# Optimization experiments

Measured on AMD Instinct MI355X. Metric: run time of the kernel, lower is better.

The kernel has to match this reference:

```python
import jax, jax.numpy as jnp
import numpy as np

NUM_EXPERTS = 8
TOP_K = 2
IN_C, HID, OUT_C, R_C = 192, 384, 192, 8
B, H, W = 4, 128, 128


def setup_inputs() -> dict:
    key = jax.random.key(0)
    ks = jax.random.split(key, 12)
    s = 0.05
    return {
        "x": jax.random.normal(ks[0], (B, IN_C, H, W), jnp.float32),
        "router_input": jax.random.normal(ks[1], (B, R_C, H, W), jnp.float32),
        "router_W": jax.random.normal(ks[2], (NUM_EXPERTS, R_C), jnp.float32) * s,
        "router_b": jnp.zeros((NUM_EXPERTS,), jnp.float32),
        "W1": jax.random.normal(ks[3], (NUM_EXPERTS, HID, IN_C), jnp.float32) * s,
        "b1": jnp.zeros((NUM_EXPERTS, HID), jnp.float32),
        "W2": jax.random.normal(ks[4], (NUM_EXPERTS, HID, HID), jnp.float32) * s,
        "b2": jnp.zeros((NUM_EXPERTS, HID), jnp.float32),
        "W3": jax.random.normal(ks[5], (NUM_EXPERTS, OUT_C, HID), jnp.float32) * (s * 0.1),
        "b3": jnp.zeros((NUM_EXPERTS, OUT_C), jnp.float32),
    }


def _gates(router_input, router_W, router_b):
    # logits: (B, E, H, W) via 1x1 conv == per-pixel linear
    logits = jnp.einsum('ec,bchw->behw', router_W, router_input) + router_b[None, :, None, None]
    lt = jnp.moveaxis(logits, 1, -1)                      # (B,H,W,E)
    _, idx = jax.lax.top_k(lt, TOP_K)                     # (B,H,W,K)
    onehot = jax.nn.one_hot(idx, NUM_EXPERTS, dtype=bool).any(axis=-2)  # (B,H,W,E)
    masked = jnp.where(onehot, lt, -jnp.inf)
    gates = jax.nn.softmax(masked, axis=-1)               # (B,H,W,E)
    return jnp.moveaxis(gates, -1, 1)                     # (B,E,H,W)


def reference(x, router_input, router_W, router_b, W1, b1, W2, b2, W3, b3):
    gates = _gates(router_input, router_W, router_b)      # (B,E,H,W)
    out = jnp.zeros((x.shape[0], OUT_C) + x.shape[2:], x.dtype)
    gelu = lambda t: jax.nn.gelu(t, approximate=False)    # torch nn.GELU is exact
    for e in range(NUM_EXPERTS):
        h1 = gelu(jnp.einsum('oc,bchw->bohw', W1[e], x) + b1[e][None, :, None, None])
        h2 = gelu(jnp.einsum('oc,bchw->bohw', W2[e], h1) + b2[e][None, :, None, None])
        y = jnp.einsum('oc,bchw->bohw', W3[e], h2) + b3[e][None, :, None, None]
        out = out + gates[:, e:e + 1] * y
    return out
```

## Files before the change

kernel.cpp:

```cpp
#include <hip/hip_runtime.h>
#include <math.h>

#define NE 8
#define IN_C 192
#define HID 384
#define OUT_C 192
#define R_C 8
#define HW 16384
#define NPIX 65536
#define PPB 16384
#define TNP 128

typedef _Float16 h8_t __attribute__((ext_vector_type(8)));
typedef float f32x4 __attribute__((ext_vector_type(4)));

__device__ __forceinline__ float gelu_exact(float v) {
  float z  = v * 0.70710678118654752f;
  float az = fabsf(z);
  float t  = __builtin_amdgcn_rcpf(1.0f + 0.3275911f * az);
  float p  = ((((1.061405429f * t - 1.453152027f) * t + 1.421413741f) * t
               - 0.284496736f) * t + 0.254829592f) * t;
  float er = 1.0f - p * __expf(-z * z);
  er = copysignf(er, z);
  return 0.5f * v * (1.0f + er);
}

__global__ __launch_bounds__(256) void router_kernel(
    const float* __restrict__ rin, const float* __restrict__ rW,
    const float* __restrict__ rb, int* __restrict__ counts,
    int* __restrict__ lists, float* __restrict__ gatev) {
  const int tid = threadIdx.x;
  const int pid = blockIdx.x * 256 + tid;
  const int img = pid >> 14;
  const int p = pid & (PPB - 1);

  __shared__ int lcount[NE];
  __shared__ int lbase[NE];
  if (tid < NE) lcount[tid] = 0;
  __syncthreads();

  const float* rbase = rin + (size_t)img * R_C * HW + p;
  float r[R_C];
#pragma unroll
  for (int c = 0; c < R_C; ++c) r[c] = rbase[(size_t)c * HW];
  float lg[NE];
#pragma unroll
  for (int e = 0; e < NE; ++e) {
    float s = rb[e];
#pragma unroll
    for (int c = 0; c < R_C; ++c) s += rW[e * R_C + c] * r[c];
    lg[e] = s;
  }
  int e0 = 0; float l0 = lg[0];
#pragma unroll
  for (int e = 1; e < NE; ++e) { if (lg[e] > l0) { l0 = lg[e]; e0 = e; } }
  int e1 = -1; float l1 = -3.4e38f;
#pragma unroll
  for (int e = 0; e < NE; ++e) {
    if (e != e0 && lg[e] > l1) { l1 = lg[e]; e1 = e; }
  }
  float ex  = expf(l1 - l0);
  float inv = 1.0f / (1.0f + ex);
  float g0 = inv, g1 = ex * inv;

  int pos0 = atomicAdd(&lcount[e0], 1);
  int pos1 = atomicAdd(&lcount[e1], 1);
  __syncthreads();
  if (tid < NE) lbase[tid] = atomicAdd(&counts[tid * 4 + img], lcount[tid]);
  __syncthreads();

  int i0 = (e0 * 4 + img) * PPB + lbase[e0] + pos0;
  lists[i0] = p;
  gatev[i0] = g0;
  int i1 = (e1 * 4 + img) * PPB + lbase[e1] + pos1;
  lists[i1] = p | (1 << 14);
  gatev[i1] = g1;
}

__global__ __launch_bounds__(256) void cvt_w1(const float* __restrict__ W,
                                              _Float16* __restrict__ d) {
  int t = blockIdx.x * 256 + threadIdx.x;
  const int QE = 73728 / 4;
  if (t >= NE * QE) return;
  int e = t / QE, q = t % QE;
  int j4 = q & 1; q >>= 1;
  int m = q % 192; q /= 192;
  int g = q % 4;   q /= 4;
  int c = q % 6;   q /= 6;
  int h = q;
  int row = h * 192 + m, col = 32 * c + 8 * g + 4 * j4;
  float4 v = *(const float4*)(W + (size_t)e * 73728 + (size_t)row * 192 + col);
  union { _Float16 h4[4]; uint2 u; } cv;
  cv.h4[0] = (_Float16)v.x; cv.h4[1] = (_Float16)v.y;
  cv.h4[2] = (_Float16)v.z; cv.h4[3] = (_Float16)v.w;
  ((uint2*)d)[t] = cv.u;
}

__global__ __launch_bounds__(256) void cvt_w2(const float* __restrict__ W,
                                              _Float16* __restrict__ d) {
  int t = blockIdx.x * 256 + threadIdx.x;
  const int QE = 147456 / 4;
  if (t >= NE * QE) return;
  int e = t / QE, q = t % QE;
  int j4 = q & 1; q >>= 1;
  int m = q % 192; q /= 192;
  int g = q % 4;   q /= 4;
  int mh = q % 2;  q /= 2;
  int c = q % 6;   q /= 6;
  int kh = q;
  int row = mh * 192 + m;
  int col = kh * 192 + 32 * c + 8 * g + 4 * j4;
  float4 v = *(const float4*)(W + (size_t)e * 147456 + (size_t)row * 384 + col);
  union { _Float16 h4[4]; uint2 u; } cv;
  cv.h4[0] = (_Float16)v.x; cv.h4[1] = (_Float16)v.y;
  cv.h4[2] = (_Float16)v.z; cv.h4[3] = (_Float16)v.w;
  ((uint2*)d)[t] = cv.u;
}

__global__ __launch_bounds__(256) void cvt_w3(const float* __restrict__ W,
                                              _Float16* __restrict__ d) {
  int t = blockIdx.x * 256 + threadIdx.x;
  const int QE = 73728 / 4;
  if (t >= NE * QE) return;
  int e = t / QE, q = t % QE;
  int j4 = q & 1; q >>= 1;
  int m = q % 192; q /= 192;
  int g = q % 4;   q /= 4;
  int c = q;
  int col = 32 * c + 8 * g + 4 * j4;
  float4 v = *(const float4*)(W + (size_t)e * 73728 + (size_t)m * 384 + col);
  union { _Float16 h4[4]; uint2 u; } cv;
  cv.h4[0] = (_Float16)v.x; cv.h4[1] = (_Float16)v.y;
  cv.h4[2] = (_Float16)v.z; cv.h4[3] = (_Float16)v.w;
  ((uint2*)d)[t] = cv.u;
}

__global__ __launch_bounds__(256) void xt_kernel(const float* __restrict__ x,
                                                 _Float16* __restrict__ xt, int pair) {
  const int img2 = blockIdx.y;
  const float* xb = x + (size_t)(pair * 2 + img2) * IN_C * HW;
  _Float16* dst = xt + (size_t)img2 * PPB * 192;
  const int tid = threadIdx.x;
  const int p = blockIdx.x * 64 + (tid & 63);
  const int cq0 = tid >> 6;
#pragma unroll
  for (int cq = 0; cq < 6; ++cq) {
    int chq = cq * 4 + cq0;
    union { _Float16 h[8]; uint4 u; } pk;
#pragma unroll
    for (int j = 0; j < 8; ++j)
      pk.h[j] = (_Float16)xb[(size_t)(chq * 8 + j) * HW + p];
    *(uint4*)(dst + (size_t)p * 192 + chq * 8) = pk.u;
  }
}

__device__ __forceinline__ void stage16(const _Float16* __restrict__ src,
                                        char* lds, int tid) {
  const int wid = tid >> 6;
  const char* g = (const char*)src;
  __builtin_amdgcn_global_load_lds(
      (const __attribute__((address_space(1))) void*)(g + tid * 16),
      (__attribute__((address_space(3))) void*)(lds + wid * 1024), 16, 0, 0);
  if (wid < 4)
    __builtin_amdgcn_global_load_lds(
        (const __attribute__((address_space(1))) void*)(g + 8192 + tid * 16),
        (__attribute__((address_space(3))) void*)(lds + 8192 + wid * 1024), 16, 0, 0);
}

__device__ __forceinline__ void pwait(int wid, bool last) {
  if (last)          asm volatile("s_waitcnt vmcnt(0)");
  else if (wid < 4)  asm volatile("s_waitcnt vmcnt(2)");
  else               asm volatile("s_waitcnt vmcnt(1)");
  __builtin_amdgcn_sched_barrier(0);
  __builtin_amdgcn_s_barrier();
  __builtin_amdgcn_sched_barrier(0);
}

__device__ __forceinline__ const _Float16* chunk_src(
    const _Float16* W1e, const _Float16* W2e, const _Float16* W3e, int cg) {
  if (cg < 6)  return W1e + cg * 6144;
  if (cg < 18) return W2e + (cg - 6) * 6144;
  if (cg < 24) return W1e + 36864 + (cg - 18) * 6144;
  if (cg < 36) return W2e + 73728 + (cg - 24) * 6144;
  return W3e + (cg - 36) * 6144;
}

template <int NM, int NT>
__device__ __forceinline__ void mfma_chunk(const _Float16* __restrict__ A,
                                           const _Float16* __restrict__ B, int kb4,
                                           int m0, int nt0,
                                           f32x4 (&acc)[NM][NT], int lane) {
  const int l15 = lane & 15, g = lane >> 4;
  h8_t a[NM], b[NT];
#pragma unroll
  for (int i = 0; i < NM; ++i)
    a[i] = *(const h8_t*)(A + ((size_t)g * 192 + m0 + i * 16 + l15) * 8);
#pragma unroll
  for (int t = 0; t < NT; ++t)
    b[t] = *(const h8_t*)(B + (((size_t)(kb4 + g) * TNP) + (nt0 + t) * 16 + l15) * 8);
#pragma unroll
  for (int i = 0; i < NM; ++i)
#pragma unroll
    for (int t = 0; t < NT; ++t)
      acc[i][t] = __builtin_amdgcn_mfma_f32_16x16x32_f16(a[i], b[t], acc[i][t], 0, 0, 0);
}

template <int NM, int NT>
__device__ __forceinline__ void act_store(f32x4 (&acc)[NM][NT], const float* __restrict__ bias,
                                          _Float16* __restrict__ Dst, int m0, int nt0, int lane) {
  const int l15 = lane & 15, g = lane >> 4;
#pragma unroll
  for (int i = 0; i < NM; ++i) {
    int rb = m0 + i * 16 + 4 * g;
    float4 bv = *(const float4*)(bias + rb);
#pragma unroll
    for (int t = 0; t < NT; ++t) {
      int n = (nt0 + t) * 16 + l15;
      union { _Float16 h[4]; uint2 u; } cv;
      cv.h[0] = (_Float16)gelu_exact(acc[i][t][0] + bv.x);
      cv.h[1] = (_Float16)gelu_exact(acc[i][t][1] + bv.y);
      cv.h[2] = (_Float16)gelu_exact(acc[i][t][2] + bv.z);
      cv.h[3] = (_Float16)gelu_exact(acc[i][t][3] + bv.w);
      *(uint2*)(Dst + (((size_t)(rb >> 3) * TNP) + n) * 8 + (rb & 7)) = cv.u;
    }
  }
}

template <int NM, int NT>
__device__ __forceinline__ void ybuf_store(f32x4 (&acc)[NM][NT], const float* __restrict__ bias,
                                           _Float16* __restrict__ ybuf,
                                           const int* __restrict__ pidsl,
                                           const float* __restrict__ pg,
                                           int npt, int m0, int nt0, int lane) {
  const int l15 = lane & 15, g = lane >> 4;
#pragma unroll
  for (int t = 0; t < NT; ++t) {
    int n = (nt0 + t) * 16 + l15;
    if (n >= npt) continue;
    float gt = pg[n];
    _Float16* yb = ybuf + pidsl[n];
#pragma unroll
    for (int i = 0; i < NM; ++i) {
      int rb = m0 + i * 16 + 4 * g;
      float4 bv = *(const float4*)(bias + rb);
      union { _Float16 h[4]; uint2 u; } cv;
      cv.h[0] = (_Float16)((acc[i][t][0] + bv.x) * gt);
      cv.h[1] = (_Float16)((acc[i][t][1] + bv.y) * gt);
      cv.h[2] = (_Float16)((acc[i][t][2] + bv.z) * gt);
      cv.h[3] = (_Float16)((acc[i][t][3] + bv.w) * gt);
      *(uint2*)(yb + rb) = cv.u;
    }
  }
}

__global__ __launch_bounds__(512, 2) void moe_mfma_kernel(
    const _Float16* __restrict__ xt,
    const _Float16* __restrict__ W1s, const float* __restrict__ b1,
    const _Float16* __restrict__ W2s, const float* __restrict__ b2,
    const _Float16* __restrict__ W3s, const float* __restrict__ b3,
    const int* __restrict__ counts, const int* __restrict__ lists,
    const float* __restrict__ gatev, _Float16* __restrict__ ybuf, int pair) {
  const int e = blockIdx.x;
  const int img2 = blockIdx.y >> 7;
  const int tile = blockIdx.y & 127;
  const int img = pair * 2 + img2;
  const int cnt = counts[e * 4 + img];
  const int start = tile * TNP;
  if (start >= cnt) return;
  const int npt = min(TNP, cnt - start);

  __shared__ __align__(16) char smem[140544];
  _Float16* XB  = (_Float16*)smem;
  _Float16* H1a = (_Float16*)(smem + 49152);
  _Float16* H2  = (_Float16*)smem;
  char* STG0 = smem + 98304;
  char* STG1 = smem + 110592;
  char* STG2 = smem + 122880;
  float* BIAS1 = (float*)(smem + 135168);
  float* BIAS2 = (float*)(smem + 136704);
  float* BIAS3 = (float*)(smem + 138240);
  int*   pp    = (int*)(smem + 139008);
  int*   pidsl = (int*)(smem + 139520);
  float* pg    = (float*)(smem + 140032);
  char* const STGp[3] = {STG0, STG1, STG2};

  const int tid = threadIdx.x;
  const int lane = tid & 63;
  const int wid = tid >> 6;
  const int m0loc = (wid >> 1) * 48;
  const int nt0 = (wid & 1) * 4;

  const _Float16* W1e = W1s + (size_t)e * 73728;
  const _Float16* W2e = W2s + (size_t)e * 147456;
  const _Float16* W3e = W3s + (size_t)e * 73728;

  if (tid < TNP) {
    int entry = 0; float g = 0.0f;
    if (tid < npt) {
      entry = lists[(e * 4 + img) * PPB + start + tid];
      g     = gatev[(e * 4 + img) * PPB + start + tid];
    }
    int p = entry & (PPB - 1);
    int slot = (entry >> 14) & 1;
    pp[tid] = img2 * PPB + p;
    pidsl[tid] = ((img2 * PPB + p) * 2 + slot) * 192;
    pg[tid] = g;
  }
  for (int i = tid; i < 960; i += 512) {
    if (i < 384) BIAS1[i] = b1[e * HID + i];
    else if (i < 768) BIAS2[i - 384] = b2[e * HID + (i - 384)];
    else BIAS3[i - 768] = b3[e * OUT_C + (i - 768)];
  }
  __syncthreads();

  for (int i = tid; i < 24 * TNP; i += 512) {
    int n = i & (TNP - 1);
    int c16 = i >> 7;
    uint4 v = {0, 0, 0, 0};
    if (n < npt) v = *(const uint4*)(xt + (size_t)pp[n] * 192 + c16 * 8);
    *(uint4*)(XB + ((size_t)c16 * TNP + n) * 8) = v;
  }
  __syncthreads();

  stage16(chunk_src(W1e, W2e, W3e, 0), STGp[0], tid);
  stage16(chunk_src(W1e, W2e, W3e, 1), STGp[1], tid);

  f32x4 acc1[3][4], acc2[6][4];
#pragma unroll
  for (int i = 0; i < 6; ++i)
#pragma unroll
    for (int t = 0; t < 4; ++t) acc2[i][t] = (f32x4){0.f, 0.f, 0.f, 0.f};

#pragma unroll
  for (int i = 0; i < 3; ++i)
#pragma unroll
    for (int t = 0; t < 4; ++t) acc1[i][t] = (f32x4){0.f, 0.f, 0.f, 0.f};
#pragma unroll
  for (int c = 0; c < 6; ++c) {
    pwait(wid, false);
    stage16(chunk_src(W1e, W2e, W3e, c + 2), STGp[(c + 2) % 3], tid);
    mfma_chunk<3, 4>((const _Float16*)STGp[c % 3], XB, c * 4, m0loc, nt0, acc1, lane);
    if (c == 5) act_store<3, 4>(acc1, BIAS1, H1a, m0loc, nt0, lane);
  }

#pragma unroll
  for (int s = 0; s < 12; ++s) {
    const int c = 6 + s;
    pwait(wid, false);
    stage16(chunk_src(W1e, W2e, W3e, c + 2), STGp[(c + 2) % 3], tid);
    const int mh = s & 1;
    f32x4 (&a2)[3][4] = *(f32x4(*)[3][4])(&acc2[mh * 3]);
    mfma_chunk<3, 4>((const _Float16*)STGp[c % 3], H1a, (s >> 1) * 4, m0loc, nt0, a2, lane);
  }

#pragma unroll
  for (int i = 0; i < 3; ++i)
#pragma unroll
    for (int t = 0; t < 4; ++t) acc1[i][t] = (f32x4){0.f, 0.f, 0.f, 0.f};
#pragma unroll
  for (int s = 0; s < 6; ++s) {
    const int c = 18 + s;
    pwait(wid, false);
    stage16(chunk_src(W1e, W2e, W3e, c + 2), STGp[(c + 2) % 3], tid);
    mfma_chunk<3, 4>((const _Float16*)STGp[c % 3], XB, s * 4, m0loc, nt0, acc1, lane);
    if (s == 5) act_store<3, 4>(acc1, BIAS1 + 192, H1a, m0loc, nt0, lane);
  }

#pragma unroll
  for (int s = 0; s < 12; ++s) {
    const int c = 24 + s;
    pwait(wid, false);
    stage16(chunk_src(W1e, W2e, W3e, c + 2), STGp[(c + 2) % 3], tid);
    const int mh = s & 1;
    f32x4 (&a2)[3][4] = *(f32x4(*)[3][4])(&acc2[mh * 3]);
    mfma_chunk<3, 4>((const _Float16*)STGp[c % 3], H1a, (s >> 1) * 4, m0loc, nt0, a2, lane);
    if (s == 11) {
      __builtin_amdgcn_sched_barrier(0);
      __builtin_amdgcn_s_barrier();
      __builtin_amdgcn_sched_barrier(0);
      f32x4 (&h0)[3][4] = *(f32x4(*)[3][4])(&acc2[0]);
      f32x4 (&h1)[3][4] = *(f32x4(*)[3][4])(&acc2[3]);
      act_store<3, 4>(h0, BIAS2, H2, m0loc, nt0, lane);
      act_store<3, 4>(h1, BIAS2, H2, 192 + m0loc, nt0, lane);
    }
  }

#pragma unroll
  for (int i = 0; i < 3; ++i)
#pragma unroll
    for (int t = 0; t < 4; ++t) acc1[i][t] = (f32x4){0.f, 0.f, 0.f, 0.f};
#pragma unroll
  for (int s = 0; s < 12; ++s) {
    const int c = 36 + s;
    pwait(wid, s == 11);
    if (c + 2 < 48) stage16(chunk_src(W1e, W2e, W3e, c + 2), STGp[(c + 2) % 3], tid);
    mfma_chunk<3, 4>((const _Float16*)STGp[c % 3], H2, s * 4, m0loc, nt0, acc1, lane);
  }

  ybuf_store<3, 4>(acc1, BIAS3, ybuf, pidsl, pg, npt, m0loc, nt0, lane);
}

__global__ __launch_bounds__(256) void sum_kernel(
    const _Float16* __restrict__ ybuf, float* __restrict__ out, int pair) {
  __shared__ float ys[64][193];
  const int tid = threadIdx.x;
  const int img2 = blockIdx.x >> 8;
  const int p0 = (blockIdx.x & 255) * 64;
  const _Float16* yb = ybuf + (size_t)(img2 * PPB + p0) * 2 * 192;

  for (int t = tid; t < 64 * 48; t += 256) {
    int p = t / 48, c4 = t % 48;
    const uint2* y0 = (const uint2*)(yb + (size_t)p * 2 * 192) + c4;
    uint2 u0 = y0[0];
    uint2 u1 = y0[48];
    union { uint2 u; _Float16 h[4]; } a, b;
    a.u = u0; b.u = u1;
#pragma unroll
    for (int j = 0; j < 4; ++j)
      ys[p][c4 * 4 + j] = (float)a.h[j] + (float)b.h[j];
  }
  __syncthreads();

  float* ob = out + (size_t)(pair * 2 + img2) * OUT_C * HW + p0;
  for (int t = tid; t < OUT_C * 64; t += 256) {
    int c = t >> 6, p = t & 63;
    ob[(size_t)c * HW + p] = ys[p][c];
  }
}

extern "C" void kernel_launch(void* const* d_in, const int* in_sizes, int n_in,
                              void* d_out, int out_size, void* d_ws, size_t ws_size,
                              hipStream_t stream) {
  const float* x   = (const float*)d_in[0];
  const float* rin = (const float*)d_in[1];
  const float* rW  = (const float*)d_in[2];
  const float* rb  = (const float*)d_in[3];
  const float* W1  = (const float*)d_in[4];
  const float* b1  = (const float*)d_in[5];
  const float* W2  = (const float*)d_in[6];
  const float* b2  = (const float*)d_in[7];
  const float* W3  = (const float*)d_in[8];
  const float* b3  = (const float*)d_in[9];
  float* out = (float*)d_out;

  char* ws = (char*)d_ws;
  int*   counts = (int*)ws;
  int*   lists  = (int*)(ws + 1024);
  float* gatev  = (float*)(ws + 1024 + (size_t)NE * 4 * PPB * 4);
  _Float16* W1s = (_Float16*)(ws + 1024 + 2 * (size_t)NE * 4 * PPB * 4);
  _Float16* W2s = W1s + (size_t)NE * HID * IN_C;
  _Float16* W3s = W2s + (size_t)NE * HID * HID;
  _Float16* ybuf = W3s + (size_t)NE * OUT_C * HID;
  _Float16* xt = ybuf + (size_t)2 * PPB * 2 * 192;

  hipMemsetAsync(counts, 0, NE * 4 * sizeof(int), stream);

  cvt_w1<<<(NE * 73728 / 4 + 255) / 256, 256, 0, stream>>>(W1, W1s);
  cvt_w2<<<(NE * 147456 / 4 + 255) / 256, 256, 0, stream>>>(W2, W2s);
  cvt_w3<<<(NE * 73728 / 4 + 255) / 256, 256, 0, stream>>>(W3, W3s);

  router_kernel<<<NPIX / 256, 256, 0, stream>>>(rin, rW, rb, counts, lists, gatev);

  for (int pair = 0; pair < 2; ++pair) {
    xt_kernel<<<dim3(PPB / 64, 2), 256, 0, stream>>>(x, xt, pair);
    moe_mfma_kernel<<<dim3(NE, 256), 512, 0, stream>>>(
        xt, W1s, b1, W2s, b2, W3s, b3, counts, lists, gatev, ybuf, pair);
    sum_kernel<<<512, 256, 0, stream>>>(ybuf, out, pair);
  }
}
```

Before: 268.2 us.

## Stream weights through a contiguous blob into a six-slot LDS ring

Merges the three weight-conversion kernels into one that writes all expert weights as a single contiguous blob in consumption order. The MFMA kernel replaces the three-buffer stage/wait scheme with a six-slot LDS ring filled by uniform 8 KB global_load_lds requests. Each phase consumes two chunks under raised wave priority and keeps more loads in flight. This aims to hide weight-load latency and cut per-chunk barrier overhead, at the cost of more shared memory (which may reduce occupancy), rolled loops and an extra barrier per phase.

```diff
diff --git a/kernel.cpp b/kernel.cpp
--- a/kernel.cpp
+++ b/kernel.cpp
@@ -77,62 +77,30 @@
   gatev[i1] = g1;
 }
 
-__global__ __launch_bounds__(256) void cvt_w1(const float* __restrict__ W,
-                                              _Float16* __restrict__ d) {
+__global__ __launch_bounds__(256) void cvt_blob(
+    const float* __restrict__ W1, const float* __restrict__ W2,
+    const float* __restrict__ W3, _Float16* __restrict__ Wb) {
   int t = blockIdx.x * 256 + threadIdx.x;
-  const int QE = 73728 / 4;
-  if (t >= NE * QE) return;
-  int e = t / QE, q = t % QE;
-  int j4 = q & 1; q >>= 1;
-  int m = q % 192; q /= 192;
-  int g = q % 4;   q /= 4;
-  int c = q % 6;   q /= 6;
-  int h = q;
-  int row = h * 192 + m, col = 32 * c + 8 * g + 4 * j4;
-  float4 v = *(const float4*)(W + (size_t)e * 73728 + (size_t)row * 192 + col);
+  if (t >= NE * 73728) return;
+  int e = t / 73728, r = t % 73728;
+  int cg = r / 1536, w = r % 1536;
+  int j4 = w & 1, gm = w >> 1;
+  int m = gm % 192, g = gm / 192;
+  const float* src; int row, col, lda;
+  if (cg < 6)       { src = W1 + (size_t)e * 73728;  row = m;       col = 32 * cg + 8 * g + 4 * j4; lda = 192; }
+  else if (cg < 18) { int s = cg - 6;  int c = s >> 1, mh = s & 1;
+                      src = W2 + (size_t)e * 147456; row = 192 * mh + m; col = 32 * c + 8 * g + 4 * j4; lda = 384; }
+  else if (cg < 24) { int c = cg - 18;
+                      src = W1 + (size_t)e * 73728;  row = 192 + m; col = 32 * c + 8 * g + 4 * j4; lda = 192; }
+  else if (cg < 36) { int s = cg - 24; int c = s >> 1, mh = s & 1;
+                      src = W2 + (size_t)e * 147456; row = 192 * mh + m; col = 192 + 32 * c + 8 * g + 4 * j4; lda = 384; }
+  else              { int c = cg - 36;
+                      src = W3 + (size_t)e * 73728;  row = m;       col = 32 * c + 8 * g + 4 * j4; lda = 384; }
+  float4 v = *(const float4*)(src + (size_t)row * lda + col);
   union { _Float16 h4[4]; uint2 u; } cv;
   cv.h4[0] = (_Float16)v.x; cv.h4[1] = (_Float16)v.y;
   cv.h4[2] = (_Float16)v.z; cv.h4[3] = (_Float16)v.w;
-  ((uint2*)d)[t] = cv.u;
-}
-
-__global__ __launch_bounds__(256) void cvt_w2(const float* __restrict__ W,
-                                              _Float16* __restrict__ d) {
-  int t = blockIdx.x * 256 + threadIdx.x;
-  const int QE = 147456 / 4;
-  if (t >= NE * QE) return;
-  int e = t / QE, q = t % QE;
-  int j4 = q & 1; q >>= 1;
-  int m = q % 192; q /= 192;
-  int g = q % 4;   q /= 4;
-  int mh = q % 2;  q /= 2;
-  int c = q % 6;   q /= 6;
-  int kh = q;
-  int row = mh * 192 + m;
-  int col = kh * 192 + 32 * c + 8 * g + 4 * j4;
-  float4 v = *(const float4*)(W + (size_t)e * 147456 + (size_t)row * 384 + col);
-  union { _Float16 h4[4]; uint2 u; } cv;
-  cv.h4[0] = (_Float16)v.x; cv.h4[1] = (_Float16)v.y;
-  cv.h4[2] = (_Float16)v.z; cv.h4[3] = (_Float16)v.w;
-  ((uint2*)d)[t] = cv.u;
-}
-
-__global__ __launch_bounds__(256) void cvt_w3(const float* __restrict__ W,
-                                              _Float16* __restrict__ d) {
-  int t = blockIdx.x * 256 + threadIdx.x;
-  const int QE = 73728 / 4;
-  if (t >= NE * QE) return;
-  int e = t / QE, q = t % QE;
-  int j4 = q & 1; q >>= 1;
-  int m = q % 192; q /= 192;
-  int g = q % 4;   q /= 4;
-  int c = q;
-  int col = 32 * c + 8 * g + 4 * j4;
-  float4 v = *(const float4*)(W + (size_t)e * 73728 + (size_t)m * 384 + col);
-  union { _Float16 h4[4]; uint2 u; } cv;
-  cv.h4[0] = (_Float16)v.x; cv.h4[1] = (_Float16)v.y;
-  cv.h4[2] = (_Float16)v.z; cv.h4[3] = (_Float16)v.w;
-  ((uint2*)d)[t] = cv.u;
+  ((uint2*)Wb)[t] = cv.u;
 }
 
 __global__ __launch_bounds__(256) void xt_kernel(const float* __restrict__ x,
@@ -154,67 +122,84 @@
   }
 }
 
-__device__ __forceinline__ void stage16(const _Float16* __restrict__ src,
-                                        char* lds, int tid) {
-  const int wid = tid >> 6;
-  const char* g = (const char*)src;
-  __builtin_amdgcn_global_load_lds(
-      (const __attribute__((address_space(1))) void*)(g + tid * 16),
-      (__attribute__((address_space(3))) void*)(lds + wid * 1024), 16, 0, 0);
-  if (wid < 4)
-    __builtin_amdgcn_global_load_lds(
-        (const __attribute__((address_space(1))) void*)(g + 8192 + tid * 16),
-        (__attribute__((address_space(3))) void*)(lds + 8192 + wid * 1024), 16, 0, 0);
-}
-
-__device__ __forceinline__ void pwait(int wid, bool last) {
-  if (last)          asm volatile("s_waitcnt vmcnt(0)");
-  else if (wid < 4)  asm volatile("s_waitcnt vmcnt(2)");
-  else               asm volatile("s_waitcnt vmcnt(1)");
+struct Pipe {
+  unsigned qi;
+  int rslot;
+  int cslot;
+  const char* wq;
+  char* RING;
+  int tid, wid;
+};
+
+__device__ __forceinline__ void pipe_issue3(Pipe& P) {
+#pragma unroll
+  for (int k = 0; k < 3; ++k) {
+    if (P.qi < 72) {
+      __builtin_amdgcn_global_load_lds(
+          (const __attribute__((address_space(1))) void*)(P.wq + P.tid * 16),
+          (__attribute__((address_space(3))) void*)(P.RING + P.rslot * 8192 + P.wid * 1024),
+          16, 0, 0);
+      P.wq += 8192;
+      P.qi++;
+      P.rslot = (P.rslot == 5) ? 0 : P.rslot + 1;
+    }
+  }
+}
+
+__device__ __forceinline__ void mfma_chunk(const _Float16* __restrict__ A,
+                                           const _Float16* __restrict__ B, int kb4,
+                                           int m0, int nt0,
+                                           f32x4 (&acc)[3][4], int lane) {
+  const int l15 = lane & 15, g = lane >> 4;
+  h8_t a[3], b[4];
+#pragma unroll
+  for (int i = 0; i < 3; ++i)
+    a[i] = *(const h8_t*)(A + ((size_t)g * 192 + m0 + i * 16 + l15) * 8);
+#pragma unroll
+  for (int t = 0; t < 4; ++t)
+    b[t] = *(const h8_t*)(B + (((size_t)(kb4 + g) * TNP) + (nt0 + t) * 16 + l15) * 8);
+#pragma unroll
+  for (int i = 0; i < 3; ++i)
+#pragma unroll
+    for (int t = 0; t < 4; ++t)
+      acc[i][t] = __builtin_amdgcn_mfma_f32_16x16x32_f16(a[i], b[t], acc[i][t], 0, 0, 0);
+}
+
+template <bool LAST, bool DRAIN>
+__device__ __forceinline__ void dphase(Pipe& P, const _Float16* __restrict__ Bsh,
+                                       int kb0, int kb1,
+                                       f32x4 (&accA)[3][4], f32x4 (&accB)[3][4],
+                                       int m0loc, int nt0, int lane) {
+  if (LAST)       asm volatile("s_waitcnt vmcnt(0)" ::: "memory");
+  else if (DRAIN) asm volatile("s_waitcnt vmcnt(3) lgkmcnt(0)" ::: "memory");
+  else            asm volatile("s_waitcnt vmcnt(3)" ::: "memory");
   __builtin_amdgcn_sched_barrier(0);
   __builtin_amdgcn_s_barrier();
   __builtin_amdgcn_sched_barrier(0);
-}
-
-__device__ __forceinline__ const _Float16* chunk_src(
-    const _Float16* W1e, const _Float16* W2e, const _Float16* W3e, int cg) {
-  if (cg < 6)  return W1e + cg * 6144;
-  if (cg < 18) return W2e + (cg - 6) * 6144;
-  if (cg < 24) return W1e + 36864 + (cg - 18) * 6144;
-  if (cg < 36) return W2e + 73728 + (cg - 24) * 6144;
-  return W3e + (cg - 36) * 6144;
-}
-
-template <int NM, int NT>
-__device__ __forceinline__ void mfma_chunk(const _Float16* __restrict__ A,
-                                           const _Float16* __restrict__ B, int kb4,
-                                           int m0, int nt0,
-                                           f32x4 (&acc)[NM][NT], int lane) {
-  const int l15 = lane & 15, g = lane >> 4;
-  h8_t a[NM], b[NT];
-#pragma unroll
-  for (int i = 0; i < NM; ++i)
-    a[i] = *(const h8_t*)(A + ((size_t)g * 192 + m0 + i * 16 + l15) * 8);
-#pragma unroll
-  for (int t = 0; t < NT; ++t)
-    b[t] = *(const h8_t*)(B + (((size_t)(kb4 + g) * TNP) + (nt0 + t) * 16 + l15) * 8);
-#pragma unroll
-  for (int i = 0; i < NM; ++i)
-#pragma unroll
-    for (int t = 0; t < NT; ++t)
-      acc[i][t] = __builtin_amdgcn_mfma_f32_16x16x32_f16(a[i], b[t], acc[i][t], 0, 0, 0);
-}
-
-template <int NM, int NT>
-__device__ __forceinline__ void act_store(f32x4 (&acc)[NM][NT], const float* __restrict__ bias,
+  const _Float16* A0 = (const _Float16*)(P.RING + P.cslot * 12288);
+  const _Float16* A1 = (const _Float16*)(P.RING + (P.cslot + 1) * 12288);
+  __builtin_amdgcn_s_setprio(1);
+  mfma_chunk(A0, Bsh, kb0, m0loc, nt0, accA, lane);
+  mfma_chunk(A1, Bsh, kb1, m0loc, nt0, accB, lane);
+  __builtin_amdgcn_s_setprio(0);
+  P.cslot ^= 2;
+  if (!LAST) {
+    __builtin_amdgcn_sched_barrier(0);
+    __builtin_amdgcn_s_barrier();
+    __builtin_amdgcn_sched_barrier(0);
+    pipe_issue3(P);
+  }
+}
+
+__device__ __forceinline__ void act_store(f32x4 (&acc)[3][4], const float* __restrict__ bias,
                                           _Float16* __restrict__ Dst, int m0, int nt0, int lane) {
   const int l15 = lane & 15, g = lane >> 4;
 #pragma unroll
-  for (int i = 0; i < NM; ++i) {
+  for (int i = 0; i < 3; ++i) {
     int rb = m0 + i * 16 + 4 * g;
     float4 bv = *(const float4*)(bias + rb);
 #pragma unroll
-    for (int t = 0; t < NT; ++t) {
+    for (int t = 0; t < 4; ++t) {
       int n = (nt0 + t) * 16 + l15;
       union { _Float16 h[4]; uint2 u; } cv;
       cv.h[0] = (_Float16)gelu_exact(acc[i][t][0] + bv.x);
@@ -226,21 +211,20 @@
   }
 }
 
-template <int NM, int NT>
-__device__ __forceinline__ void ybuf_store(f32x4 (&acc)[NM][NT], const float* __restrict__ bias,
+__device__ __forceinline__ void ybuf_store(f32x4 (&acc)[3][4], const float* __restrict__ bias,
                                            _Float16* __restrict__ ybuf,
                                            const int* __restrict__ pidsl,
                                            const float* __restrict__ pg,
                                            int npt, int m0, int nt0, int lane) {
   const int l15 = lane & 15, g = lane >> 4;
 #pragma unroll
-  for (int t = 0; t < NT; ++t) {
+  for (int t = 0; t < 4; ++t) {
     int n = (nt0 + t) * 16 + l15;
     if (n >= npt) continue;
     float gt = pg[n];
     _Float16* yb = ybuf + pidsl[n];
 #pragma unroll
-    for (int i = 0; i < NM; ++i) {
+    for (int i = 0; i < 3; ++i) {
       int rb = m0 + i * 16 + 4 * g;
       float4 bv = *(const float4*)(bias + rb);
       union { _Float16 h[4]; uint2 u; } cv;
@@ -254,10 +238,9 @@
 }
 
 __global__ __launch_bounds__(512, 2) void moe_mfma_kernel(
-    const _Float16* __restrict__ xt,
-    const _Float16* __restrict__ W1s, const float* __restrict__ b1,
-    const _Float16* __restrict__ W2s, const float* __restrict__ b2,
-    const _Float16* __restrict__ W3s, const float* __restrict__ b3,
+    const _Float16* __restrict__ xt, const _Float16* __restrict__ Wb,
+    const float* __restrict__ b1, const float* __restrict__ b2,
+    const float* __restrict__ b3,
     const int* __restrict__ counts, const int* __restrict__ lists,
     const float* __restrict__ gatev, _Float16* __restrict__ ybuf, int pair) {
   const int e = blockIdx.x;
@@ -269,30 +252,23 @@
   if (start >= cnt) return;
   const int npt = min(TNP, cnt - start);
 
-  __shared__ __align__(16) char smem[140544];
+  __shared__ __align__(16) char smem[152832];
   _Float16* XB  = (_Float16*)smem;
   _Float16* H1a = (_Float16*)(smem + 49152);
   _Float16* H2  = (_Float16*)smem;
-  char* STG0 = smem + 98304;
-  char* STG1 = smem + 110592;
-  char* STG2 = smem + 122880;
-  float* BIAS1 = (float*)(smem + 135168);
-  float* BIAS2 = (float*)(smem + 136704);
-  float* BIAS3 = (float*)(smem + 138240);
-  int*   pp    = (int*)(smem + 139008);
-  int*   pidsl = (int*)(smem + 139520);
-  float* pg    = (float*)(smem + 140032);
-  char* const STGp[3] = {STG0, STG1, STG2};
+  char* RING   = smem + 98304;
+  float* BIAS1 = (float*)(smem + 147456);
+  float* BIAS2 = (float*)(smem + 148992);
+  float* BIAS3 = (float*)(smem + 150528);
+  int*   pp    = (int*)(smem + 151296);
+  int*   pidsl = (int*)(smem + 151808);
+  float* pg    = (float*)(smem + 152320);
 
   const int tid = threadIdx.x;
   const int lane = tid & 63;
   const int wid = tid >> 6;
   const int m0loc = (wid >> 1) * 48;
   const int nt0 = (wid & 1) * 4;
-
-  const _Float16* W1e = W1s + (size_t)e * 73728;
-  const _Float16* W2e = W2s + (size_t)e * 147456;
-  const _Float16* W3e = W3s + (size_t)e * 73728;
 
   if (tid < TNP) {
     int entry = 0; float g = 0.0f;
@@ -322,82 +298,57 @@
   }
   __syncthreads();
 
-  stage16(chunk_src(W1e, W2e, W3e, 0), STGp[0], tid);
-  stage16(chunk_src(W1e, W2e, W3e, 1), STGp[1], tid);
-
-  f32x4 acc1[3][4], acc2[6][4];
-#pragma unroll
-  for (int i = 0; i < 6; ++i)
-#pragma unroll
-    for (int t = 0; t < 4; ++t) acc2[i][t] = (f32x4){0.f, 0.f, 0.f, 0.f};
-
+  Pipe P{0u, 0, 0, (const char*)(Wb + (size_t)e * 294912), RING, tid, wid};
+  pipe_issue3(P);
+  pipe_issue3(P);
+
+  f32x4 acc1[3][4], acc2a[3][4], acc2b[3][4];
 #pragma unroll
   for (int i = 0; i < 3; ++i)
 #pragma unroll
+    for (int t = 0; t < 4; ++t) {
+      acc1[i][t] = (f32x4){0.f, 0.f, 0.f, 0.f};
+      acc2a[i][t] = (f32x4){0.f, 0.f, 0.f, 0.f};
+      acc2b[i][t] = (f32x4){0.f, 0.f, 0.f, 0.f};
+    }
+
+#pragma unroll 1
+  for (int s = 0; s < 3; ++s)
+    dphase<false, false>(P, XB, 8 * s, 8 * s + 4, acc1, acc1, m0loc, nt0, lane);
+  act_store(acc1, BIAS1, H1a, m0loc, nt0, lane);
+
+  dphase<false, true>(P, H1a, 0, 0, acc2a, acc2b, m0loc, nt0, lane);
+#pragma unroll 1
+  for (int s = 1; s < 6; ++s)
+    dphase<false, false>(P, H1a, 4 * s, 4 * s, acc2a, acc2b, m0loc, nt0, lane);
+
+#pragma unroll
+  for (int i = 0; i < 3; ++i)
+#pragma unroll
     for (int t = 0; t < 4; ++t) acc1[i][t] = (f32x4){0.f, 0.f, 0.f, 0.f};
-#pragma unroll
-  for (int c = 0; c < 6; ++c) {
-    pwait(wid, false);
-    stage16(chunk_src(W1e, W2e, W3e, c + 2), STGp[(c + 2) % 3], tid);
-    mfma_chunk<3, 4>((const _Float16*)STGp[c % 3], XB, c * 4, m0loc, nt0, acc1, lane);
-    if (c == 5) act_store<3, 4>(acc1, BIAS1, H1a, m0loc, nt0, lane);
-  }
-
-#pragma unroll
-  for (int s = 0; s < 12; ++s) {
-    const int c = 6 + s;
-    pwait(wid, false);
-    stage16(chunk_src(W1e, W2e, W3e, c + 2), STGp[(c + 2) % 3], tid);
-    const int mh = s & 1;
-    f32x4 (&a2)[3][4] = *(f32x4(*)[3][4])(&acc2[mh * 3]);
-    mfma_chunk<3, 4>((const _Float16*)STGp[c % 3], H1a, (s >> 1) * 4, m0loc, nt0, a2, lane);
-  }
+#pragma unroll 1
+  for (int s = 0; s < 3; ++s)
+    dphase<false, false>(P, XB, 8 * s, 8 * s + 4, acc1, acc1, m0loc, nt0, lane);
+  act_store(acc1, BIAS1 + 192, H1a, m0loc, nt0, lane);
+
+  dphase<false, true>(P, H1a, 0, 0, acc2a, acc2b, m0loc, nt0, lane);
+#pragma unroll 1
+  for (int s = 1; s < 6; ++s)
+    dphase<false, false>(P, H1a, 4 * s, 4 * s, acc2a, acc2b, m0loc, nt0, lane);
+  act_store(acc2a, BIAS2, H2, m0loc, nt0, lane);
+  act_store(acc2b, BIAS2, H2, 192 + m0loc, nt0, lane);
 
 #pragma unroll
   for (int i = 0; i < 3; ++i)
 #pragma unroll
     for (int t = 0; t < 4; ++t) acc1[i][t] = (f32x4){0.f, 0.f, 0.f, 0.f};
-#pragma unroll
-  for (int s = 0; s < 6; ++s) {
-    const int c = 18 + s;
-    pwait(wid, false);
-    stage16(chunk_src(W1e, W2e, W3e, c + 2), STGp[(c + 2) % 3], tid);
-    mfma_chunk<3, 4>((const _Float16*)STGp[c % 3], XB, s * 4, m0loc, nt0, acc1, lane);
-    if (s == 5) act_store<3, 4>(acc1, BIAS1 + 192, H1a, m0loc, nt0, lane);
-  }
-
-#pragma unroll
-  for (int s = 0; s < 12; ++s) {
-    const int c = 24 + s;
-    pwait(wid, false);
-    stage16(chunk_src(W1e, W2e, W3e, c + 2), STGp[(c + 2) % 3], tid);
-    const int mh = s & 1;
-    f32x4 (&a2)[3][4] = *(f32x4(*)[3][4])(&acc2[mh * 3]);
-    mfma_chunk<3, 4>((const _Float16*)STGp[c % 3], H1a, (s >> 1) * 4, m0loc, nt0, a2, lane);
-    if (s == 11) {
-      __builtin_amdgcn_sched_barrier(0);
-      __builtin_amdgcn_s_barrier();
-      __builtin_amdgcn_sched_barrier(0);
-      f32x4 (&h0)[3][4] = *(f32x4(*)[3][4])(&acc2[0]);
-      f32x4 (&h1)[3][4] = *(f32x4(*)[3][4])(&acc2[3]);
-      act_store<3, 4>(h0, BIAS2, H2, m0loc, nt0, lane);
-      act_store<3, 4>(h1, BIAS2, H2, 192 + m0loc, nt0, lane);
-    }
-  }
-
-#pragma unroll
-  for (int i = 0; i < 3; ++i)
-#pragma unroll
-    for (int t = 0; t < 4; ++t) acc1[i][t] = (f32x4){0.f, 0.f, 0.f, 0.f};
-#pragma unroll
-  for (int s = 0; s < 12; ++s) {
-    const int c = 36 + s;
-    pwait(wid, s == 11);
-    if (c + 2 < 48) stage16(chunk_src(W1e, W2e, W3e, c + 2), STGp[(c + 2) % 3], tid);
-    mfma_chunk<3, 4>((const _Float16*)STGp[c % 3], H2, s * 4, m0loc, nt0, acc1, lane);
-  }
-
-  ybuf_store<3, 4>(acc1, BIAS3, ybuf, pidsl, pg, npt, m0loc, nt0, lane);
+  dphase<false, true>(P, H2, 0, 4, acc1, acc1, m0loc, nt0, lane);
+#pragma unroll 1
+  for (int s = 1; s < 5; ++s)
+    dphase<false, false>(P, H2, 8 * s, 8 * s + 4, acc1, acc1, m0loc, nt0, lane);
+  dphase<true, false>(P, H2, 40, 44, acc1, acc1, m0loc, nt0, lane);
+
+  ybuf_store(acc1, BIAS3, ybuf, pidsl, pg, npt, m0loc, nt0, lane);
 }
 
 __global__ __launch_bounds__(256) void sum_kernel(
@@ -447,24 +398,20 @@
   int*   counts = (int*)ws;
   int*   lists  = (int*)(ws + 1024);
   float* gatev  = (float*)(ws + 1024 + (size_t)NE * 4 * PPB * 4);
-  _Float16* W1s = (_Float16*)(ws + 1024 + 2 * (size_t)NE * 4 * PPB * 4);
-  _Float16* W2s = W1s + (size_t)NE * HID * IN_C;
-  _Float16* W3s = W2s + (size_t)NE * HID * HID;
-  _Float16* ybuf = W3s + (size_t)NE * OUT_C * HID;
+  _Float16* Wb  = (_Float16*)(ws + 1024 + 2 * (size_t)NE * 4 * PPB * 4);
+  _Float16* ybuf = Wb + (size_t)NE * 294912;
   _Float16* xt = ybuf + (size_t)2 * PPB * 2 * 192;
 
   hipMemsetAsync(counts, 0, NE * 4 * sizeof(int), stream);
 
-  cvt_w1<<<(NE * 73728 / 4 + 255) / 256, 256, 0, stream>>>(W1, W1s);
-  cvt_w2<<<(NE * 147456 / 4 + 255) / 256, 256, 0, stream>>>(W2, W2s);
-  cvt_w3<<<(NE * 73728 / 4 + 255) / 256, 256, 0, stream>>>(W3, W3s);
+  cvt_blob<<<(NE * 73728 + 255) / 256, 256, 0, stream>>>(W1, W2, W3, Wb);
 
   router_kernel<<<NPIX / 256, 256, 0, stream>>>(rin, rW, rb, counts, lists, gatev);
 
   for (int pair = 0; pair < 2; ++pair) {
     xt_kernel<<<dim3(PPB / 64, 2), 256, 0, stream>>>(x, xt, pair);
     moe_mfma_kernel<<<dim3(NE, 256), 512, 0, stream>>>(
-        xt, W1s, b1, W2s, b2, W3s, b3, counts, lists, gatev, ybuf, pair);
+        xt, Wb, b1, b2, b3, counts, lists, gatev, ybuf, pair);
     sum_kernel<<<512, 256, 0, stream>>>(ybuf, out, pair);
   }
 }
```

New measurement: 262.6 us. -2.1%, faster.
